# Kernel optimization log

Measured on AMD Instinct MI355X. Metric: run time of the kernel, lower is better.

Reference implementation:

```python
import jax, jax.numpy as jnp
import numpy as np

IN, H, STEPS = 4, 64, 5

def setup_inputs() -> dict:
    key = jax.random.key(0)
    ks = jax.random.split(key, 12)
    s = 1.0 / np.sqrt(H)
    def u(k, shape):
        return jax.random.uniform(k, shape, jnp.float32, -s, s)
    return {
        "x":    jax.random.normal(ks[0], (4096, 512, IN), jnp.float32),
        "Wih0": u(ks[1], (4 * H, IN)),
        "Whh0": u(ks[2], (4 * H, H)),
        "bih0": u(ks[3], (4 * H,)),
        "bhh0": u(ks[4], (4 * H,)),
        "Wih1": u(ks[5], (4 * H, H)),
        "Whh1": u(ks[6], (4 * H, H)),
        "bih1": u(ks[7], (4 * H,)),
        "bhh1": u(ks[8], (4 * H,)),
        "Wfc":  u(ks[9], (IN * STEPS, H)),
        "bfc":  u(ks[10], (IN * STEPS,)),
    }

def _lstm_layer(x, Wih, Whh, bih, bhh, collect):
    # x: [B, T, in]; PyTorch gate order: i, f, g, o
    B = x.shape[0]
    xg = jnp.einsum('bti,gi->tbg', x, Wih) + bih  # precompute input gates [T,B,4H]
    h0 = jnp.zeros((B, H), x.dtype)
    c0 = jnp.zeros((B, H), x.dtype)

    def step(carry, xg_t):
        h, c = carry
        gates = xg_t + h @ Whh.T + bhh  # [B,4H]
        i, f, g, o = jnp.split(gates, 4, axis=-1)
        i = jax.nn.sigmoid(i); f = jax.nn.sigmoid(f)
        g = jnp.tanh(g);       o = jax.nn.sigmoid(o)
        c = f * c + i * g
        h = o * jnp.tanh(c)
        return (h, c), (h if collect else None)

    (h_last, _), ys = jax.lax.scan(step, (h0, c0), xg)
    return ys, h_last  # ys: [T,B,H] (or None)

def reference(x, Wih0, Whh0, bih0, bhh0, Wih1, Whh1, bih1, bhh1, Wfc, bfc):
    ys1, _ = _lstm_layer(x, Wih0, Whh0, bih0, bhh0, collect=True)   # [T,B,H]
    x2 = jnp.transpose(ys1, (1, 0, 2))                               # [B,T,H]
    _, h_last = _lstm_layer(x2, Wih1, Whh1, bih1, bhh1, collect=False)
    out = h_last @ Wfc.T + bfc                                       # [B, IN*STEPS]
    return out.reshape(-1, STEPS, IN)
```

## Files before the change

kernel.cpp:

```cpp
#include <hip/hip_runtime.h>
#include <hip/hip_bf16.h>
#include <cstdint>

#define BLOCK 512
#define BT 16
#define RS_H 136
#define RS_F 68
#define XS   2052

typedef __attribute__((ext_vector_type(8))) short bf16x8;
typedef __attribute__((ext_vector_type(4))) float f32x4;
typedef __attribute__((ext_vector_type(2))) float f32x2;
typedef __attribute__((ext_vector_type(2))) unsigned int u32x2;
typedef __attribute__((ext_vector_type(4))) unsigned int u32x4;

#define LOG2E 1.44269504f

static __device__ __forceinline__ float exp2_fast(float x) {
#if __has_builtin(__builtin_amdgcn_exp2f)
    return __builtin_amdgcn_exp2f(x);
#else
    return __expf(x * 0.69314718056f);
#endif
}
static __device__ __forceinline__ float rcp_fast(float x) {
    return __builtin_amdgcn_rcpf(x);
}
static __device__ __forceinline__ unsigned short f2bf(float f) {
    union { float f; unsigned u; } v; v.f = f;
    unsigned r = v.u + 0x7fffu + ((v.u >> 16) & 1u);
    return (unsigned short)(r >> 16);
}
static __device__ __forceinline__ bf16x8 load_wfrag(const float* __restrict__ w, int off, float scale) {
    union { bf16x8 v; unsigned short s[8]; } u;
#pragma unroll
    for (int j = 0; j < 8; ++j) u.s[j] = f2bf(w[off + j] * scale);
    return u.v;
}

extern "C" __global__ void __launch_bounds__(BLOCK, 2)
lstm_fused6(const float* __restrict__ x,
            const float* __restrict__ Wih0, const float* __restrict__ Whh0,
            const float* __restrict__ bih0, const float* __restrict__ bhh0,
            const float* __restrict__ Wih1, const float* __restrict__ Whh1,
            const float* __restrict__ bih1, const float* __restrict__ bhh1,
            const float* __restrict__ Wfc,  const float* __restrict__ bfc,
            float* __restrict__ out)
{
    __shared__ unsigned short hbuf[2][BT * RS_H];
    __shared__ float hfin[BT * RS_F];
    __shared__ unsigned short xlds[BT * XS + 8];

    const int tid   = threadIdx.x;
    const int b0    = blockIdx.x * BT;
    const int lane  = tid & 63;
    const int wv    = tid >> 6;
    const int layer = wv >> 2;
    const int cb    = (wv & 3) * 16;
    const int n16   = lane & 15;
    const int quad  = lane >> 4;

    for (int i = tid; i < 2 * BT * RS_H; i += BLOCK)
        ((unsigned short*)hbuf)[i] = 0;

    for (int i = tid; i < BT * 512; i += BLOCK) {
        const int r = i >> 9, t = i & 511;
        const f32x4 xv = *(const f32x4*)(x + ((size_t)(b0 + r) * 2048 + t * 4));
        const unsigned lo = (unsigned)f2bf(xv[0]) | ((unsigned)f2bf(xv[1]) << 16);
        const unsigned hi = (unsigned)f2bf(xv[2]) | ((unsigned)f2bf(xv[3]) << 16);
        *(u32x2*)&xlds[r * XS + t * 4] = (u32x2){lo, hi};
    }
    if (tid <= BT) {
        const int off = (tid < BT) ? tid * XS + 2048 : BT * XS;
        *(u32x2*)&xlds[off] = (u32x2){0u, 0u};
    }

    const float gsc[4] = {-LOG2E, -LOG2E, 2.0f * LOG2E, -LOG2E};

    bf16x8 wf[4][4];
    f32x4  biasv[4];
    if (layer == 0) {
#pragma unroll
        for (int g = 0; g < 4; ++g) {
            const int gc = g * 64 + cb + n16;
            const float s = gsc[g];
            wf[g][0] = load_wfrag(Whh0 + gc * 64, quad * 8, s);
            wf[g][1] = load_wfrag(Whh0 + gc * 64, 32 + quad * 8, s);
            union { bf16x8 v; unsigned short s_[8]; } u;
#pragma unroll
            for (int c = 0; c < 4; ++c)
                u.s_[c] = (quad == 0) ? f2bf(Wih0[gc * 4 + c] * s) : (unsigned short)0;
            u.s_[4] = 0; u.s_[5] = 0; u.s_[6] = 0; u.s_[7] = 0;
            wf[g][2] = u.v;
            const int gb = g * 64 + cb + quad * 4;
#pragma unroll
            for (int r = 0; r < 4; ++r)
                biasv[g][r] = (bih0[gb + r] + bhh0[gb + r]) * s;
        }
    } else {
#pragma unroll
        for (int g = 0; g < 4; ++g) {
            const int gc = g * 64 + cb + n16;
            const float s = gsc[g];
            wf[g][0] = load_wfrag(Wih1 + gc * 64, quad * 8, s);
            wf[g][1] = load_wfrag(Wih1 + gc * 64, 32 + quad * 8, s);
            wf[g][2] = load_wfrag(Whh1 + gc * 64, quad * 8, s);
            wf[g][3] = load_wfrag(Whh1 + gc * 64, 32 + quad * 8, s);
            const int gb = g * 64 + cb + quad * 4;
#pragma unroll
            for (int r = 0; r < 4; ++r)
                biasv[g][r] = (bih1[gb + r] + bhh1[gb + r]) * s;
        }
    }

    float cst[4] = {0.f, 0.f, 0.f, 0.f};

    int xoff = (quad == 0) ? n16 * XS : BT * XS;
    const int xadv = (quad == 0) ? 4 : 0;

    const int rbase = n16 * RS_H + quad * 8;
    const int wbase = n16 * RS_H + layer * 64 + cb + quad * 4;
    const unsigned short* __restrict__ rdp0 = &hbuf[1][rbase];
    const unsigned short* __restrict__ rdp1 = &hbuf[0][rbase];
    unsigned short* __restrict__ wrp0 = &hbuf[0][wbase];
    unsigned short* __restrict__ wrp1 = &hbuf[1][wbase];
    float* __restrict__ hfp = &hfin[n16 * RS_F + cb + quad * 4];

    const f32x2 onev  = {1.0f, 1.0f};
    const f32x2 k2l   = {2.0f * LOG2E, 2.0f * LOG2E};
    const f32x2 km2l  = {-2.0f * LOG2E, -2.0f * LOG2E};
    const f32x2 cclmp = {60.0f, 60.0f};

    __syncthreads();

    auto step = [&](const unsigned short* __restrict__ rp,
                    unsigned short* __restrict__ wp,
                    bool l0act, bool l1act, bool fin) __attribute__((always_inline)) {
        f32x4 acc[4];
        if (layer == 0) {
            if (l0act) {
                const bf16x8 s0 = *(const bf16x8*)(rp);
                const bf16x8 s1 = *(const bf16x8*)(rp + 32);
                const u32x2 xr = *(const u32x2*)&xlds[xoff];
                xoff += xadv;
                const u32x4 xt = {xr.x, xr.y, 0u, 0u};
                const bf16x8 sx = __builtin_bit_cast(bf16x8, xt);
#pragma unroll
                for (int g = 0; g < 4; ++g) {
                    acc[g] = __builtin_amdgcn_mfma_f32_16x16x32_bf16(wf[g][0], s0, biasv[g], 0, 0, 0);
                    acc[g] = __builtin_amdgcn_mfma_f32_16x16x32_bf16(wf[g][1], s1, acc[g], 0, 0, 0);
                    acc[g] = __builtin_amdgcn_mfma_f32_16x16x32_bf16(wf[g][2], sx, acc[g], 0, 0, 0);
                }
            }
        } else {
            if (l1act) {
                const bf16x8 s0 = *(const bf16x8*)(rp);
                const bf16x8 s1 = *(const bf16x8*)(rp + 32);
                const bf16x8 s2 = *(const bf16x8*)(rp + 64);
                const bf16x8 s3 = *(const bf16x8*)(rp + 96);
#pragma unroll
                for (int g = 0; g < 4; ++g) {
                    acc[g] = __builtin_amdgcn_mfma_f32_16x16x32_bf16(wf[g][0], s0, biasv[g], 0, 0, 0);
                    acc[g] = __builtin_amdgcn_mfma_f32_16x16x32_bf16(wf[g][1], s1, acc[g], 0, 0, 0);
                    acc[g] = __builtin_amdgcn_mfma_f32_16x16x32_bf16(wf[g][2], s2, acc[g], 0, 0, 0);
                    acc[g] = __builtin_amdgcn_mfma_f32_16x16x32_bf16(wf[g][3], s3, acc[g], 0, 0, 0);
                }
            }
        }
        const bool act = layer ? l1act : l0act;
        if (act) {
            unsigned hw0 = 0, hw1 = 0;
            float hf0 = 0.f, hf1 = 0.f, hf2 = 0.f, hf3 = 0.f;
#pragma unroll
            for (int p = 0; p < 2; ++p) {
                const f32x2 ei = {exp2_fast(acc[0][2*p]), exp2_fast(acc[0][2*p+1])};
                const f32x2 ef = {exp2_fast(acc[1][2*p]), exp2_fast(acc[1][2*p+1])};
                const f32x2 eg = {exp2_fast(acc[2][2*p]), exp2_fast(acc[2][2*p+1])};
                const f32x2 eo = {exp2_fast(acc[3][2*p]), exp2_fast(acc[3][2*p+1])};

                const f32x2 t2 = __builtin_elementwise_fma(eg, k2l, km2l);
                const f32x2 d1 = (eg + onev) * (ei + onev);
                const f32x2 df = ef + onev;
                const f32x2 pr = d1 * df;
                const f32x2 R  = {rcp_fast(pr[0]), rcp_fast(pr[1])};
                const f32x2 P  = t2 * R * df;
                const f32x2 fv = R * d1;

                f32x2 cp = {cst[2*p], cst[2*p+1]};
                f32x2 c2 = __builtin_elementwise_fma(fv, cp, P);
                c2 = __builtin_elementwise_min(c2, cclmp);
                cst[2*p] = c2[0]; cst[2*p+1] = c2[1];

                const f32x2 ec = {exp2_fast(c2[0]), exp2_fast(c2[1])};
                const f32x2 d2 = (ec + onev) * (eo + onev);
                const f32x2 r2 = {rcp_fast(d2[0]), rcp_fast(d2[1])};
                const f32x2 h  = (ec - onev) * r2;

                union { __hip_bfloat162 b; unsigned u; } hb;
                hb.b = __float22bfloat162_rn(make_float2(h[0], h[1]));
                if (p == 0) { hw0 = hb.u; hf0 = h[0]; hf1 = h[1]; }
                else        { hw1 = hb.u; hf2 = h[0]; hf3 = h[1]; }
            }
            *(u32x2*)wp = (u32x2){hw0, hw1};
            if (fin && layer == 1)
                *(f32x4*)hfp = (f32x4){hf0, hf1, hf2, hf3};
        }
        __syncthreads();
    };

    step(rdp0, wrp0, true,  false, false);
    for (int k = 0; k < 255; ++k) {
        step(rdp1, wrp1, true, true, false);
        step(rdp0, wrp0, true, true, false);
    }
    step(rdp1, wrp1, true,  true,  false);
    step(rdp0, wrp0, false, true,  true);

    if (tid < BT * 20) {
        const int m = tid / 20, k = tid % 20;
        float acc = bfc[k];
#pragma unroll 8
        for (int j = 0; j < 64; ++j)
            acc += hfin[m * RS_F + j] * Wfc[k * 64 + j];
        out[(b0 + m) * 20 + k] = acc;
    }
}

extern "C" void kernel_launch(void* const* d_in, const int* in_sizes, int n_in,
                              void* d_out, int out_size, void* d_ws, size_t ws_size,
                              hipStream_t stream)
{
    (void)in_sizes; (void)n_in; (void)d_ws; (void)ws_size; (void)out_size;
    const float* xp    = (const float*)d_in[0];
    const float* Wih0p = (const float*)d_in[1];
    const float* Whh0p = (const float*)d_in[2];
    const float* bih0p = (const float*)d_in[3];
    const float* bhh0p = (const float*)d_in[4];
    const float* Wih1p = (const float*)d_in[5];
    const float* Whh1p = (const float*)d_in[6];
    const float* bih1p = (const float*)d_in[7];
    const float* bhh1p = (const float*)d_in[8];
    const float* Wfcp  = (const float*)d_in[9];
    const float* bfcp  = (const float*)d_in[10];

    lstm_fused6<<<dim3(256), dim3(BLOCK), 0, stream>>>(
        xp, Wih0p, Whh0p, bih0p, bhh0p, Wih1p, Whh1p, bih1p, bhh1p,
        Wfcp, bfcp, (float*)d_out);
}
```

Baseline: 417.1 us.

## Halve block to 4 waves, each computing two 16-column gate tiles per step

Cuts the block from 8 to 4 wavefronts, so each wave now handles 32 hidden columns (two 16-wide tiles) per layer and issues twice as many MFMAs per step. The per-step __syncthreads now spans fewer waves, and the doubled independent MFMA chains give more ILP within each wave. It also prefetches the next x fragment from LDS one step ahead. The trade-off is roughly double the register pressure per wave (weights and accumulators) and more serial work per wave on the recurrent critical path.

```diff
diff --git a/kernel.cpp b/kernel.cpp
--- a/kernel.cpp
+++ b/kernel.cpp
@@ -2,7 +2,7 @@
 #include <hip/hip_bf16.h>
 #include <cstdint>
 
-#define BLOCK 512
+#define BLOCK 256
 #define BT 16
 #define RS_H 136
 #define RS_F 68
@@ -38,14 +38,14 @@
     return u.v;
 }
 
-extern "C" __global__ void __launch_bounds__(BLOCK, 2)
-lstm_fused6(const float* __restrict__ x,
-            const float* __restrict__ Wih0, const float* __restrict__ Whh0,
-            const float* __restrict__ bih0, const float* __restrict__ bhh0,
-            const float* __restrict__ Wih1, const float* __restrict__ Whh1,
-            const float* __restrict__ bih1, const float* __restrict__ bhh1,
-            const float* __restrict__ Wfc,  const float* __restrict__ bfc,
-            float* __restrict__ out)
+extern "C" __global__ void __launch_bounds__(BLOCK, 1)
+lstm_fused10(const float* __restrict__ x,
+             const float* __restrict__ Wih0, const float* __restrict__ Whh0,
+             const float* __restrict__ bih0, const float* __restrict__ bhh0,
+             const float* __restrict__ Wih1, const float* __restrict__ Whh1,
+             const float* __restrict__ bih1, const float* __restrict__ bhh1,
+             const float* __restrict__ Wfc,  const float* __restrict__ bfc,
+             float* __restrict__ out)
 {
     __shared__ unsigned short hbuf[2][BT * RS_H];
     __shared__ float hfin[BT * RS_F];
@@ -55,8 +55,8 @@
     const int b0    = blockIdx.x * BT;
     const int lane  = tid & 63;
     const int wv    = tid >> 6;
-    const int layer = wv >> 2;
-    const int cb    = (wv & 3) * 16;
+    const int layer = wv >> 1;
+    const int cb    = (wv & 1) * 32;
     const int n16   = lane & 15;
     const int quad  = lane >> 4;
 
@@ -77,43 +77,47 @@
 
     const float gsc[4] = {-LOG2E, -LOG2E, 2.0f * LOG2E, -LOG2E};
 
-    bf16x8 wf[4][4];
-    f32x4  biasv[4];
+    bf16x8 wf[2][4][4];
+    f32x4  biasv[2][4];
     if (layer == 0) {
 #pragma unroll
+        for (int u = 0; u < 2; ++u)
+#pragma unroll
         for (int g = 0; g < 4; ++g) {
-            const int gc = g * 64 + cb + n16;
+            const int gc = g * 64 + cb + u * 16 + n16;
             const float s = gsc[g];
-            wf[g][0] = load_wfrag(Whh0 + gc * 64, quad * 8, s);
-            wf[g][1] = load_wfrag(Whh0 + gc * 64, 32 + quad * 8, s);
-            union { bf16x8 v; unsigned short s_[8]; } u;
+            wf[u][g][0] = load_wfrag(Whh0 + gc * 64, quad * 8, s);
+            wf[u][g][1] = load_wfrag(Whh0 + gc * 64, 32 + quad * 8, s);
+            union { bf16x8 v; unsigned short s_[8]; } uu;
 #pragma unroll
             for (int c = 0; c < 4; ++c)
-                u.s_[c] = (quad == 0) ? f2bf(Wih0[gc * 4 + c] * s) : (unsigned short)0;
-            u.s_[4] = 0; u.s_[5] = 0; u.s_[6] = 0; u.s_[7] = 0;
-            wf[g][2] = u.v;
-            const int gb = g * 64 + cb + quad * 4;
+                uu.s_[c] = (quad == 0) ? f2bf(Wih0[gc * 4 + c] * s) : (unsigned short)0;
+            uu.s_[4] = 0; uu.s_[5] = 0; uu.s_[6] = 0; uu.s_[7] = 0;
+            wf[u][g][2] = uu.v;
+            const int gb = g * 64 + cb + u * 16 + quad * 4;
 #pragma unroll
             for (int r = 0; r < 4; ++r)
-                biasv[g][r] = (bih0[gb + r] + bhh0[gb + r]) * s;
+                biasv[u][g][r] = (bih0[gb + r] + bhh0[gb + r]) * s;
         }
     } else {
 #pragma unroll
+        for (int u = 0; u < 2; ++u)
+#pragma unroll
         for (int g = 0; g < 4; ++g) {
-            const int gc = g * 64 + cb + n16;
+            const int gc = g * 64 + cb + u * 16 + n16;
             const float s = gsc[g];
-            wf[g][0] = load_wfrag(Wih1 + gc * 64, quad * 8, s);
-            wf[g][1] = load_wfrag(Wih1 + gc * 64, 32 + quad * 8, s);
-            wf[g][2] = load_wfrag(Whh1 + gc * 64, quad * 8, s);
-            wf[g][3] = load_wfrag(Whh1 + gc * 64, 32 + quad * 8, s);
-            const int gb = g * 64 + cb + quad * 4;
+            wf[u][g][0] = load_wfrag(Wih1 + gc * 64, quad * 8, s);
+            wf[u][g][1] = load_wfrag(Wih1 + gc * 64, 32 + quad * 8, s);
+            wf[u][g][2] = load_wfrag(Whh1 + gc * 64, quad * 8, s);
+            wf[u][g][3] = load_wfrag(Whh1 + gc * 64, 32 + quad * 8, s);
+            const int gb = g * 64 + cb + u * 16 + quad * 4;
 #pragma unroll
             for (int r = 0; r < 4; ++r)
-                biasv[g][r] = (bih1[gb + r] + bhh1[gb + r]) * s;
-        }
-    }
-
-    float cst[4] = {0.f, 0.f, 0.f, 0.f};
+                biasv[u][g][r] = (bih1[gb + r] + bhh1[gb + r]) * s;
+        }
+    }
+
+    f32x2 cst2[2][2] = {{{0.f,0.f},{0.f,0.f}}, {{0.f,0.f},{0.f,0.f}}};
 
     int xoff = (quad == 0) ? n16 * XS : BT * XS;
     const int xadv = (quad == 0) ? 4 : 0;
@@ -133,23 +137,28 @@
 
     __syncthreads();
 
+    u32x2 xcur = {0u, 0u};
+    if (layer == 0) { xcur = *(const u32x2*)&xlds[xoff]; xoff += xadv; }
+
     auto step = [&](const unsigned short* __restrict__ rp,
                     unsigned short* __restrict__ wp,
                     bool l0act, bool l1act, bool fin) __attribute__((always_inline)) {
-        f32x4 acc[4];
+        f32x4 acc[2][4];
         if (layer == 0) {
             if (l0act) {
                 const bf16x8 s0 = *(const bf16x8*)(rp);
                 const bf16x8 s1 = *(const bf16x8*)(rp + 32);
-                const u32x2 xr = *(const u32x2*)&xlds[xoff];
+                const u32x4 xt = {xcur.x, xcur.y, 0u, 0u};
+                const bf16x8 sx = __builtin_bit_cast(bf16x8, xt);
+                xcur = *(const u32x2*)&xlds[xoff];
                 xoff += xadv;
-                const u32x4 xt = {xr.x, xr.y, 0u, 0u};
-                const bf16x8 sx = __builtin_bit_cast(bf16x8, xt);
+#pragma unroll
+                for (int u = 0; u < 2; ++u)
 #pragma unroll
                 for (int g = 0; g < 4; ++g) {
-                    acc[g] = __builtin_amdgcn_mfma_f32_16x16x32_bf16(wf[g][0], s0, biasv[g], 0, 0, 0);
-                    acc[g] = __builtin_amdgcn_mfma_f32_16x16x32_bf16(wf[g][1], s1, acc[g], 0, 0, 0);
-                    acc[g] = __builtin_amdgcn_mfma_f32_16x16x32_bf16(wf[g][2], sx, acc[g], 0, 0, 0);
+                    acc[u][g] = __builtin_amdgcn_mfma_f32_16x16x32_bf16(wf[u][g][0], s0, biasv[u][g], 0, 0, 0);
+                    acc[u][g] = __builtin_amdgcn_mfma_f32_16x16x32_bf16(wf[u][g][1], s1, acc[u][g], 0, 0, 0);
+                    acc[u][g] = __builtin_amdgcn_mfma_f32_16x16x32_bf16(wf[u][g][2], sx, acc[u][g], 0, 0, 0);
                 }
             }
         } else {
@@ -159,51 +168,55 @@
                 const bf16x8 s2 = *(const bf16x8*)(rp + 64);
                 const bf16x8 s3 = *(const bf16x8*)(rp + 96);
 #pragma unroll
+                for (int u = 0; u < 2; ++u)
+#pragma unroll
                 for (int g = 0; g < 4; ++g) {
-                    acc[g] = __builtin_amdgcn_mfma_f32_16x16x32_bf16(wf[g][0], s0, biasv[g], 0, 0, 0);
-                    acc[g] = __builtin_amdgcn_mfma_f32_16x16x32_bf16(wf[g][1], s1, acc[g], 0, 0, 0);
-                    acc[g] = __builtin_amdgcn_mfma_f32_16x16x32_bf16(wf[g][2], s2, acc[g], 0, 0, 0);
-                    acc[g] = __builtin_amdgcn_mfma_f32_16x16x32_bf16(wf[g][3], s3, acc[g], 0, 0, 0);
+                    acc[u][g] = __builtin_amdgcn_mfma_f32_16x16x32_bf16(wf[u][g][0], s0, biasv[u][g], 0, 0, 0);
+                    acc[u][g] = __builtin_amdgcn_mfma_f32_16x16x32_bf16(wf[u][g][1], s1, acc[u][g], 0, 0, 0);
+                    acc[u][g] = __builtin_amdgcn_mfma_f32_16x16x32_bf16(wf[u][g][2], s2, acc[u][g], 0, 0, 0);
+                    acc[u][g] = __builtin_amdgcn_mfma_f32_16x16x32_bf16(wf[u][g][3], s3, acc[u][g], 0, 0, 0);
                 }
             }
         }
         const bool act = layer ? l1act : l0act;
         if (act) {
-            unsigned hw0 = 0, hw1 = 0;
-            float hf0 = 0.f, hf1 = 0.f, hf2 = 0.f, hf3 = 0.f;
-#pragma unroll
-            for (int p = 0; p < 2; ++p) {
-                const f32x2 ei = {exp2_fast(acc[0][2*p]), exp2_fast(acc[0][2*p+1])};
-                const f32x2 ef = {exp2_fast(acc[1][2*p]), exp2_fast(acc[1][2*p+1])};
-                const f32x2 eg = {exp2_fast(acc[2][2*p]), exp2_fast(acc[2][2*p+1])};
-                const f32x2 eo = {exp2_fast(acc[3][2*p]), exp2_fast(acc[3][2*p+1])};
-
-                const f32x2 t2 = __builtin_elementwise_fma(eg, k2l, km2l);
-                const f32x2 d1 = (eg + onev) * (ei + onev);
-                const f32x2 df = ef + onev;
-                const f32x2 pr = d1 * df;
-                const f32x2 R  = {rcp_fast(pr[0]), rcp_fast(pr[1])};
-                const f32x2 P  = t2 * R * df;
-                const f32x2 fv = R * d1;
-
-                f32x2 cp = {cst[2*p], cst[2*p+1]};
-                f32x2 c2 = __builtin_elementwise_fma(fv, cp, P);
-                c2 = __builtin_elementwise_min(c2, cclmp);
-                cst[2*p] = c2[0]; cst[2*p+1] = c2[1];
-
-                const f32x2 ec = {exp2_fast(c2[0]), exp2_fast(c2[1])};
-                const f32x2 d2 = (ec + onev) * (eo + onev);
-                const f32x2 r2 = {rcp_fast(d2[0]), rcp_fast(d2[1])};
-                const f32x2 h  = (ec - onev) * r2;
-
-                union { __hip_bfloat162 b; unsigned u; } hb;
-                hb.b = __float22bfloat162_rn(make_float2(h[0], h[1]));
-                if (p == 0) { hw0 = hb.u; hf0 = h[0]; hf1 = h[1]; }
-                else        { hw1 = hb.u; hf2 = h[0]; hf3 = h[1]; }
+#pragma unroll
+            for (int u = 0; u < 2; ++u) {
+                unsigned hw0 = 0, hw1 = 0;
+                float hf0 = 0.f, hf1 = 0.f, hf2 = 0.f, hf3 = 0.f;
+#pragma unroll
+                for (int p = 0; p < 2; ++p) {
+                    const f32x2 ei = {exp2_fast(acc[u][0][2*p]), exp2_fast(acc[u][0][2*p+1])};
+                    const f32x2 ef = {exp2_fast(acc[u][1][2*p]), exp2_fast(acc[u][1][2*p+1])};
+                    const f32x2 eg = {exp2_fast(acc[u][2][2*p]), exp2_fast(acc[u][2][2*p+1])};
+                    const f32x2 eo = {exp2_fast(acc[u][3][2*p]), exp2_fast(acc[u][3][2*p+1])};
+
+                    const f32x2 t2 = __builtin_elementwise_fma(eg, k2l, km2l);
+                    const f32x2 d1 = (eg + onev) * (ei + onev);
+                    const f32x2 df = ef + onev;
+                    const f32x2 pr = d1 * df;
+                    const f32x2 R  = {rcp_fast(pr[0]), rcp_fast(pr[1])};
+                    const f32x2 P  = t2 * R * df;
+                    const f32x2 fv = R * d1;
+
+                    f32x2 c2 = __builtin_elementwise_fma(fv, cst2[u][p], P);
+                    c2 = __builtin_elementwise_min(c2, cclmp);
+                    cst2[u][p] = c2;
+
+                    const f32x2 ec = {exp2_fast(c2[0]), exp2_fast(c2[1])};
+                    const f32x2 d2 = (ec + onev) * (eo + onev);
+                    const f32x2 r2 = {rcp_fast(d2[0]), rcp_fast(d2[1])};
+                    const f32x2 h  = (ec - onev) * r2;
+
+                    union { __hip_bfloat162 b; unsigned w; } hb;
+                    hb.b = __float22bfloat162_rn(make_float2(h[0], h[1]));
+                    if (p == 0) { hw0 = hb.w; hf0 = h[0]; hf1 = h[1]; }
+                    else        { hw1 = hb.w; hf2 = h[0]; hf3 = h[1]; }
+                }
+                *(u32x2*)(wp + u * 16) = (u32x2){hw0, hw1};
+                if (fin && layer == 1)
+                    *(f32x4*)(hfp + u * 16) = (f32x4){hf0, hf1, hf2, hf3};
             }
-            *(u32x2*)wp = (u32x2){hw0, hw1};
-            if (fin && layer == 1)
-                *(f32x4*)hfp = (f32x4){hf0, hf1, hf2, hf3};
         }
         __syncthreads();
     };
@@ -216,8 +229,8 @@
     step(rdp1, wrp1, true,  true,  false);
     step(rdp0, wrp0, false, true,  true);
 
-    if (tid < BT * 20) {
-        const int m = tid / 20, k = tid % 20;
+    for (int o = tid; o < BT * 20; o += BLOCK) {
+        const int m = o / 20, k = o % 20;
         float acc = bfc[k];
 #pragma unroll 8
         for (int j = 0; j < 64; ++j)
@@ -243,7 +256,7 @@
     const float* Wfcp  = (const float*)d_in[9];
     const float* bfcp  = (const float*)d_in[10];
 
-    lstm_fused6<<<dim3(256), dim3(BLOCK), 0, stream>>>(
+    lstm_fused10<<<dim3(256), dim3(BLOCK), 0, stream>>>(
         xp, Wih0p, Whh0p, bih0p, bhh0p, Wih1p, Whh1p, bih1p, bhh1p,
         Wfcp, bfcp, (float*)d_out);
 }
```

Result: slower. 529.8 us (+27.0%).

## Duplicate MFMA waves to split LSTM gate activation work across two sub-waves

Applied to the files above, without the earlier changes.

Doubles the block to 1024 threads. Each role wave is duplicated: both copies compute the same MFMA gate accumulators, but each handles the pointwise activations and cell update for only half of the accumulator elements. This shortens the serial per-step activation chain that sits between barriers. In exchange, MFMA work and weight registers per CU are duplicated, and the per-step __syncthreads now spans twice as many waves.

```diff
diff --git a/kernel.cpp b/kernel.cpp
--- a/kernel.cpp
+++ b/kernel.cpp
@@ -2,7 +2,7 @@
 #include <hip/hip_bf16.h>
 #include <cstdint>
 
-#define BLOCK 512
+#define BLOCK 1024
 #define BT 16
 #define RS_H 136
 #define RS_F 68
@@ -38,14 +38,14 @@
     return u.v;
 }
 
-extern "C" __global__ void __launch_bounds__(BLOCK, 2)
-lstm_fused6(const float* __restrict__ x,
-            const float* __restrict__ Wih0, const float* __restrict__ Whh0,
-            const float* __restrict__ bih0, const float* __restrict__ bhh0,
-            const float* __restrict__ Wih1, const float* __restrict__ Whh1,
-            const float* __restrict__ bih1, const float* __restrict__ bhh1,
-            const float* __restrict__ Wfc,  const float* __restrict__ bfc,
-            float* __restrict__ out)
+extern "C" __global__ void __launch_bounds__(BLOCK, 4)
+lstm_fused11(const float* __restrict__ x,
+             const float* __restrict__ Wih0, const float* __restrict__ Whh0,
+             const float* __restrict__ bih0, const float* __restrict__ bhh0,
+             const float* __restrict__ Wih1, const float* __restrict__ Whh1,
+             const float* __restrict__ bih1, const float* __restrict__ bhh1,
+             const float* __restrict__ Wfc,  const float* __restrict__ bfc,
+             float* __restrict__ out)
 {
     __shared__ unsigned short hbuf[2][BT * RS_H];
     __shared__ float hfin[BT * RS_F];
@@ -55,8 +55,10 @@
     const int b0    = blockIdx.x * BT;
     const int lane  = tid & 63;
     const int wv    = tid >> 6;
-    const int layer = wv >> 2;
-    const int cb    = (wv & 3) * 16;
+    const int role  = wv & 7;
+    const int sub   = wv >> 3;
+    const int layer = role >> 2;
+    const int cb    = (role & 3) * 16;
     const int n16   = lane & 15;
     const int quad  = lane >> 4;
 
@@ -113,18 +115,18 @@
         }
     }
 
-    float cst[4] = {0.f, 0.f, 0.f, 0.f};
+    f32x2 cst = {0.f, 0.f};
 
     int xoff = (quad == 0) ? n16 * XS : BT * XS;
     const int xadv = (quad == 0) ? 4 : 0;
 
     const int rbase = n16 * RS_H + quad * 8;
-    const int wbase = n16 * RS_H + layer * 64 + cb + quad * 4;
+    const int wbase = n16 * RS_H + layer * 64 + cb + quad * 4 + sub * 2;
     const unsigned short* __restrict__ rdp0 = &hbuf[1][rbase];
     const unsigned short* __restrict__ rdp1 = &hbuf[0][rbase];
     unsigned short* __restrict__ wrp0 = &hbuf[0][wbase];
     unsigned short* __restrict__ wrp1 = &hbuf[1][wbase];
-    float* __restrict__ hfp = &hfin[n16 * RS_F + cb + quad * 4];
+    float* __restrict__ hfp = &hfin[n16 * RS_F + cb + quad * 4 + sub * 2];
 
     const f32x2 onev  = {1.0f, 1.0f};
     const f32x2 k2l   = {2.0f * LOG2E, 2.0f * LOG2E};
@@ -169,41 +171,41 @@
         }
         const bool act = layer ? l1act : l0act;
         if (act) {
-            unsigned hw0 = 0, hw1 = 0;
-            float hf0 = 0.f, hf1 = 0.f, hf2 = 0.f, hf3 = 0.f;
-#pragma unroll
-            for (int p = 0; p < 2; ++p) {
-                const f32x2 ei = {exp2_fast(acc[0][2*p]), exp2_fast(acc[0][2*p+1])};
-                const f32x2 ef = {exp2_fast(acc[1][2*p]), exp2_fast(acc[1][2*p+1])};
-                const f32x2 eg = {exp2_fast(acc[2][2*p]), exp2_fast(acc[2][2*p+1])};
-                const f32x2 eo = {exp2_fast(acc[3][2*p]), exp2_fast(acc[3][2*p+1])};
-
-                const f32x2 t2 = __builtin_elementwise_fma(eg, k2l, km2l);
-                const f32x2 d1 = (eg + onev) * (ei + onev);
-                const f32x2 df = ef + onev;
-                const f32x2 pr = d1 * df;
-                const f32x2 R  = {rcp_fast(pr[0]), rcp_fast(pr[1])};
-                const f32x2 P  = t2 * R * df;
-                const f32x2 fv = R * d1;
-
-                f32x2 cp = {cst[2*p], cst[2*p+1]};
-                f32x2 c2 = __builtin_elementwise_fma(fv, cp, P);
-                c2 = __builtin_elementwise_min(c2, cclmp);
-                cst[2*p] = c2[0]; cst[2*p+1] = c2[1];
-
-                const f32x2 ec = {exp2_fast(c2[0]), exp2_fast(c2[1])};
-                const f32x2 d2 = (ec + onev) * (eo + onev);
-                const f32x2 r2 = {rcp_fast(d2[0]), rcp_fast(d2[1])};
-                const f32x2 h  = (ec - onev) * r2;
-
-                union { __hip_bfloat162 b; unsigned u; } hb;
-                hb.b = __float22bfloat162_rn(make_float2(h[0], h[1]));
-                if (p == 0) { hw0 = hb.u; hf0 = h[0]; hf1 = h[1]; }
-                else        { hw1 = hb.u; hf2 = h[0]; hf3 = h[1]; }
+            f32x2 ai, af, ag, ao;
+            if (sub == 0) {
+                ai = (f32x2){acc[0][0], acc[0][1]}; af = (f32x2){acc[1][0], acc[1][1]};
+                ag = (f32x2){acc[2][0], acc[2][1]}; ao = (f32x2){acc[3][0], acc[3][1]};
+            } else {
+                ai = (f32x2){acc[0][2], acc[0][3]}; af = (f32x2){acc[1][2], acc[1][3]};
+                ag = (f32x2){acc[2][2], acc[2][3]}; ao = (f32x2){acc[3][2], acc[3][3]};
             }
-            *(u32x2*)wp = (u32x2){hw0, hw1};
+            const f32x2 ei = {exp2_fast(ai[0]), exp2_fast(ai[1])};
+            const f32x2 ef = {exp2_fast(af[0]), exp2_fast(af[1])};
+            const f32x2 eg = {exp2_fast(ag[0]), exp2_fast(ag[1])};
+            const f32x2 eo = {exp2_fast(ao[0]), exp2_fast(ao[1])};
+
+            const f32x2 t2 = __builtin_elementwise_fma(eg, k2l, km2l);
+            const f32x2 d1 = (eg + onev) * (ei + onev);
+            const f32x2 df = ef + onev;
+            const f32x2 pr = d1 * df;
+            const f32x2 R  = {rcp_fast(pr[0]), rcp_fast(pr[1])};
+            const f32x2 P  = t2 * R * df;
+            const f32x2 fv = R * d1;
+
+            f32x2 c2 = __builtin_elementwise_fma(fv, cst, P);
+            c2 = __builtin_elementwise_min(c2, cclmp);
+            cst = c2;
+
+            const f32x2 ec = {exp2_fast(c2[0]), exp2_fast(c2[1])};
+            const f32x2 d2 = (ec + onev) * (eo + onev);
+            const f32x2 r2 = {rcp_fast(d2[0]), rcp_fast(d2[1])};
+            const f32x2 h  = (ec - onev) * r2;
+
+            union { __hip_bfloat162 b; unsigned u; } hb;
+            hb.b = __float22bfloat162_rn(make_float2(h[0], h[1]));
+            *(unsigned*)wp = hb.u;
             if (fin && layer == 1)
-                *(f32x4*)hfp = (f32x4){hf0, hf1, hf2, hf3};
+                *(f32x2*)hfp = h;
         }
         __syncthreads();
     };
@@ -243,7 +245,7 @@
     const float* Wfcp  = (const float*)d_in[9];
     const float* bfcp  = (const float*)d_in[10];
 
-    lstm_fused6<<<dim3(256), dim3(BLOCK), 0, stream>>>(
+    lstm_fused11<<<dim3(256), dim3(BLOCK), 0, stream>>>(
         xp, Wih0p, Whh0p, bih0p, bhh0p, Wih1p, Whh1p, bih1p, bhh1p,
         Wfcp, bfcp, (float*)d_out);
 }
```

Result: slower. 517.3 us (+24.0%).
